# Kernel optimization log

Hardware: AMD Instinct MI355X
Metric: run time of the kernel (lower is better)

The kernel has to match this reference:

```python
import jax, jax.numpy as jnp
import numpy as np

IOU_THRESHOLD = 0.5
CLASS_CONF_THRESHOLD = 0.01
MAX_OUTPUT = 100  # tf.image.non_max_suppression max_output_size


def _nms_indices(boxes, scores, max_out, iou_thr):
    """Fixed-size greedy NMS: returns (idxs[max_out], valid[max_out])."""
    x1, y1, x2, y2 = boxes[:, 0], boxes[:, 1], boxes[:, 2], boxes[:, 3]
    areas = (x2 - x1) * (y2 - y1)

    def body(sc, _):
        i = jnp.argmax(sc)
        valid = sc[i] > 0.0  # score_threshold = 0.0 in tf call
        xx1 = jnp.maximum(x1[i], x1)
        yy1 = jnp.maximum(y1[i], y1)
        xx2 = jnp.minimum(x2[i], x2)
        yy2 = jnp.minimum(y2[i], y2)
        inter = jnp.maximum(xx2 - xx1, 0.0) * jnp.maximum(yy2 - yy1, 0.0)
        union = areas[i] + areas - inter
        iou = jnp.where(union > 0.0, inter / union, 0.0)
        # suppress overlapping boxes (self included, iou=1) only if pick valid
        sc_new = jnp.where((iou > iou_thr) & valid, -1.0, sc)
        return sc_new, (i, valid)

    _, (idxs, valids) = jax.lax.scan(body, scores, None, length=max_out)
    return idxs, valids


def _decode(x, anchors):
    B, H, W, A, C = x.shape  # B == 1
    gw = jnp.float32(W)
    # grid offsets: (col, row) per cell, matching cell_x / transposed cell_y
    cx = jnp.broadcast_to(jnp.arange(W, dtype=jnp.float32).reshape(1, 1, W, 1, 1), (1, H, W, 1, 1))
    cy = jnp.broadcast_to(jnp.arange(H, dtype=jnp.float32).reshape(1, H, 1, 1, 1), (1, H, W, 1, 1))
    grid = jnp.concatenate([cx, cy], axis=-1)  # (1,H,W,1,2)

    xy = (jax.nn.sigmoid(x[..., 0:2]) + grid) / gw                      # (B,H,W,A,2)
    wh = jnp.exp(x[..., 2:4]) * anchors.reshape(1, 1, 1, A, 2) / gw     # (B,H,W,A,2)
    boxes = jnp.concatenate([xy - wh / 2.0, xy + wh / 2.0], axis=-1)    # (B,H,W,A,4)

    conf = jax.nn.sigmoid(x[..., 4:5])                                  # (B,H,W,A,1)
    cls_prob = jax.nn.softmax(x[..., 5:], axis=-1)                      # (B,H,W,A,C-5)
    class_confidence = conf * cls_prob
    masked = jnp.where(class_confidence > CLASS_CONF_THRESHOLD, class_confidence, 0.0)
    classes = jnp.argmax(masked, axis=-1).astype(jnp.int32)             # (B,H,W,A)
    confm = jnp.max(masked, axis=-1)                                    # (B,H,W,A)

    N = H * W * A
    return boxes.reshape(N, 4), confm.reshape(N), classes.reshape(N)


def reference(x, anchors):
    boxes, scores, classes = _decode(x, anchors)
    idxs, valids = _nms_indices(jax.lax.stop_gradient(boxes),
                                jax.lax.stop_gradient(scores),
                                MAX_OUTPUT, IOU_THRESHOLD)
    sel_conf = jnp.where(valids, scores[idxs], 0.0)
    sel_boxes = jnp.where(valids[:, None], boxes[idxs], 0.0)
    sel_classes = jnp.where(valids, classes[idxs], -1)
    return sel_conf, sel_boxes, sel_classes


def setup_inputs() -> dict:
    key = jax.random.key(0)
    k1, k2 = jax.random.split(key)
    x = jax.random.normal(k1, (1, 256, 256, 5, 85), dtype=jnp.float32)
    # anchor priors in grid units (positive widths/heights)
    anchors = jax.random.uniform(k2, (5, 2), dtype=jnp.float32) * 4.0 + 0.5
    return {"x": x, "anchors": anchors}
```

## Files before the change

kernel.cpp:

```cpp
#include <hip/hip_runtime.h>
#include <hip/hip_bf16.h>

#define NROW 327680
#define NCLS 80
#define K_TARGET 1024u
#define CAP 2048u
#define MAX_OUT 100
#define NBIN 864
#define BIN0 0x3C23

#define WS_SCORES 0
#define WS_HIST   1310720
#define WS_CNT    1314176
#define WS_KEYS   1314240

typedef __attribute__((address_space(1))) const unsigned int g_uint;
typedef __attribute__((address_space(3))) unsigned int lds_uint;

__device__ __forceinline__ void async_copy16(const float* g, float* l) {
  __builtin_amdgcn_global_load_lds((const g_uint*)g, (lds_uint*)l, 16, 0, 0);
}

__global__ __launch_bounds__(64) void decode_score(
    const float* __restrict__ x, float* __restrict__ scores) {
  __shared__ float lds[64 * 85];
  const int t = threadIdx.x;
  const int row0 = blockIdx.x * 64;
  const float* gbase = x + (size_t)row0 * 85;

  #pragma unroll
  for (int i = 0; i < 21; ++i) {
    const int idx = i * 64 + t;
    async_copy16(gbase + idx * 4, lds + idx * 4);
  }
  if (t < 16) {
    const int idx = 1344 + t;
    async_copy16(gbase + idx * 4, lds + idx * 4);
  }
  __syncthreads();

  const float* row = lds + t * 85;
  float m = row[5];
  for (int c = 1; c < NCLS; ++c) { float l = row[5 + c]; if (l > m) m = l; }
  float s = 0.f;
  for (int c = 0; c < NCLS; ++c) s += expf(row[5 + c] - m);
  float conf = 1.f / (1.f + expf(-row[4]));
  float p = 1.f / s;
  float best = conf * p;
  scores[row0 + t] = (best > 0.01f) ? best : 0.f;
}

__global__ __launch_bounds__(1024) void hist_kernel(
    const float* __restrict__ scores, unsigned* __restrict__ hist) {
  __shared__ unsigned h[NBIN];
  const int t = threadIdx.x;
  if (t < NBIN) h[t] = 0;
  __syncthreads();

  float4 s4 = ((const float4*)scores)[blockIdx.x * 1024 + t];
  float sv[4] = {s4.x, s4.y, s4.z, s4.w};
  #pragma unroll
  for (int k = 0; k < 4; ++k) {
    float s = sv[k];
    if (s > 0.f) {
      int idx = (int)(__float_as_uint(s) >> 16) - BIN0;
      if (idx > NBIN - 1) idx = NBIN - 1;
      atomicAdd(&h[idx], 1u);
    }
  }
  __syncthreads();
  if (t < NBIN && h[t]) atomicAdd(&hist[t], h[t]);
}

__global__ __launch_bounds__(1024) void thresh_kernel(
    const unsigned* __restrict__ hist, unsigned* __restrict__ cnt) {
  __shared__ unsigned bufA[1024], bufB[1024];
  const int t = threadIdx.x;
  bufA[t] = (t < NBIN) ? hist[t] : 0u;
  __syncthreads();
  unsigned* src = bufA; unsigned* dst = bufB;
  for (int d = 1; d < 1024; d <<= 1) {
    unsigned val = src[t] + ((t + d < 1024) ? src[t + d] : 0u);
    dst[t] = val;
    __syncthreads();
    unsigned* tmp = src; src = dst; dst = tmp;
  }
  if (src[t] >= K_TARGET && (t == 1023 || src[t + 1] < K_TARGET)) {
    unsigned T = (unsigned)t;
    if (src[t] > CAP) T += 1;
    cnt[1] = T;
  }
  if (t == 0 && src[0] < K_TARGET) cnt[1] = 0;
}

__global__ __launch_bounds__(256) void compact_kernel(
    const float* __restrict__ scores, unsigned* __restrict__ cnt,
    unsigned long long* __restrict__ keys) {
  __shared__ unsigned blocal, bbase;
  const int t = threadIdx.x;
  if (t == 0) blocal = 0;
  __syncthreads();

  const unsigned T = cnt[1];
  const int gi = blockIdx.x * 256 + t;
  float4 s4 = ((const float4*)scores)[gi];
  float sv[4] = {s4.x, s4.y, s4.z, s4.w};
  unsigned long long lk[4]; int nl = 0;
  #pragma unroll
  for (int k = 0; k < 4; ++k) {
    float s = sv[k];
    if (s <= 0.f) continue;
    unsigned bits = __float_as_uint(s);
    int idx = (int)(bits >> 16) - BIN0;
    if (idx > NBIN - 1) idx = NBIN - 1;
    if ((unsigned)idx < T) continue;
    unsigned r = (unsigned)(gi * 4 + k);
    lk[nl++] = ((unsigned long long)bits << 32) |
               (unsigned long long)(0xFFFFFFFFu - r);
  }
  unsigned lpos = nl ? atomicAdd(&blocal, (unsigned)nl) : 0u;
  __syncthreads();
  if (t == 0 && blocal) bbase = atomicAdd(&cnt[0], blocal);
  __syncthreads();
  if (nl) {
    unsigned base = bbase + lpos;
    for (int i = 0; i < nl; ++i)
      if (base + i < CAP) keys[base + i] = lk[i];
  }
}

__global__ __launch_bounds__(1024) void final_kernel(
    const float* __restrict__ x, const float* __restrict__ anchors,
    const unsigned* __restrict__ cnt, const unsigned long long* __restrict__ keys,
    float* __restrict__ out) {
  __shared__ unsigned long long sk[CAP];
  __shared__ float4 cbox[CAP];
  __shared__ float4 kbox[MAX_OUT];
  __shared__ float  kscore[MAX_OUT];
  __shared__ int    krow[MAX_OUT];
  __shared__ int    knum;
  const int t = threadIdx.x;
  if (t == 0) knum = 0;

  unsigned n = cnt[0]; if (n > CAP) n = CAP;
  unsigned npow2 = 2; while (npow2 < n) npow2 <<= 1;
  for (unsigned i = t; i < npow2; i += 1024) sk[i] = (i < n) ? keys[i] : 0ull;
  __syncthreads();

  for (unsigned k = 2; k <= npow2; k <<= 1) {
    for (unsigned j = k >> 1; j > 0; j >>= 1) {
      for (unsigned i = t; i < npow2; i += 1024) {
        unsigned ixj = i ^ j;
        if (ixj > i) {
          unsigned long long a = sk[i], b = sk[ixj];
          bool desc = ((i & k) == 0);
          if (desc ? (a < b) : (a > b)) { sk[i] = b; sk[ixj] = a; }
        }
      }
      __syncthreads();
    }
  }

  for (unsigned i = t; i < n; i += 1024) {
    unsigned r = 0xFFFFFFFFu - (unsigned)(sk[i] & 0xFFFFFFFFull);
    const float* rp = x + (size_t)r * 85;
    float tx = rp[0], ty = rp[1], tw = rp[2], th = rp[3];
    const int a  = (int)(r % 5u);
    const int hw = (int)(r / 5u);
    const float wf = (float)(hw & 255);
    const float hf = (float)(hw >> 8);
    float sx = 1.f / (1.f + expf(-tx));
    float sy = 1.f / (1.f + expf(-ty));
    float xc = (sx + wf) / 256.f;
    float yc = (sy + hf) / 256.f;
    float bw = expf(tw) * anchors[2*a]     / 256.f;
    float bh = expf(th) * anchors[2*a + 1] / 256.f;
    float hwd = bw / 2.f, hhd = bh / 2.f;
    cbox[i] = make_float4(xc - hwd, yc - hhd, xc + hwd, yc + hhd);
  }
  __syncthreads();

  if (t < 64) {
    int nk = 0;
    float ax1=0,ay1=0,ax2=0,ay2=0,aar=0;
    float bx1=0,by1=0,bx2=0,by2=0,bar=0;
    for (unsigned cc = 0; cc < n && nk < MAX_OUT; ++cc) {
      unsigned long long key = sk[cc];
      unsigned sbits = (unsigned)(key >> 32);
      if (sbits == 0u) break;
      float4 bb = cbox[cc];
      float area = (bb.z - bb.x) * (bb.w - bb.y);
      bool s0 = false, s1 = false;
      if (t < nk) {
        float xx1 = fmaxf(ax1, bb.x), yy1 = fmaxf(ay1, bb.y);
        float xx2 = fminf(ax2, bb.z), yy2 = fminf(ay2, bb.w);
        float inter = fmaxf(xx2 - xx1, 0.f) * fmaxf(yy2 - yy1, 0.f);
        float uni = aar + area - inter;
        s0 = (uni > 0.f) && (inter / uni > 0.5f);
      }
      if (t + 64 < nk) {
        float xx1 = fmaxf(bx1, bb.x), yy1 = fmaxf(by1, bb.y);
        float xx2 = fminf(bx2, bb.z), yy2 = fminf(by2, bb.w);
        float inter = fmaxf(xx2 - xx1, 0.f) * fmaxf(yy2 - yy1, 0.f);
        float uni = bar + area - inter;
        s1 = (uni > 0.f) && (inter / uni > 0.5f);
      }
      if (!__any(s0 || s1)) {
        if (t == nk)      { ax1=bb.x; ay1=bb.y; ax2=bb.z; ay2=bb.w; aar=area; }
        if (t == nk - 64) { bx1=bb.x; by1=bb.y; bx2=bb.z; by2=bb.w; bar=area; }
        if (t == 0) {
          unsigned r = 0xFFFFFFFFu - (unsigned)(key & 0xFFFFFFFFull);
          kbox[nk] = bb; kscore[nk] = __uint_as_float(sbits); krow[nk] = (int)r;
        }
        ++nk;
      }
    }
    if (t == 0) knum = nk;
  }
  __syncthreads();

  if (t < MAX_OUT) {
    float conf = 0.f; float4 bb = make_float4(0.f, 0.f, 0.f, 0.f); float cf = -1.f;
    if (t < knum) {
      conf = kscore[t]; bb = kbox[t];
      const float* rp = x + (size_t)krow[t] * 85;
      float m = rp[5]; int am = 0;
      for (int c = 1; c < NCLS; ++c) { float l = rp[5 + c]; if (l > m) { m = l; am = c; } }
      cf = (float)am;
    }
    out[t] = conf;
    ((float4*)(out + 100))[t] = bb;
    out[500 + t] = cf;
  }
}

extern "C" void kernel_launch(void* const* d_in, const int* in_sizes, int n_in,
                              void* d_out, int out_size, void* d_ws, size_t ws_size,
                              hipStream_t stream) {
  const float* x       = (const float*)d_in[0];
  const float* anchors = (const float*)d_in[1];
  float* out = (float*)d_out;
  char* ws = (char*)d_ws;

  float*              scores = (float*)(ws + WS_SCORES);
  unsigned*           hist   = (unsigned*)(ws + WS_HIST);
  unsigned*           cnt    = (unsigned*)(ws + WS_CNT);
  unsigned long long* keys   = (unsigned long long*)(ws + WS_KEYS);

  hipMemsetAsync(hist, 0, NBIN * sizeof(unsigned) + 64, stream);

  hipLaunchKernelGGL(decode_score, dim3(NROW / 64), dim3(64),
                     0, stream, x, scores);
  hipLaunchKernelGGL(hist_kernel, dim3(NROW / 4096), dim3(1024),
                     0, stream, scores, hist);
  hipLaunchKernelGGL(thresh_kernel, dim3(1), dim3(1024), 0, stream, hist, cnt);
  hipLaunchKernelGGL(compact_kernel, dim3(NROW / 1024), dim3(256),
                     0, stream, scores, cnt, keys);
  hipLaunchKernelGGL(final_kernel, dim3(1), dim3(1024), 0, stream,
                     x, anchors, cnt, keys, out);
}
```

Baseline: 249.3 us.

## Register-load decode rows, per-block histograms, halve bitonic threads, parallel class argmax

The decode kernel stops staging rows through LDS with async copies and instead has each thread load its 85-float row straight into registers using unaligned vector loads, at 256 threads per block. Histogram blocks write per-block partials that the threshold kernel sums, which drops the memset and global atomics; the threshold kernel now also resets the compaction counter. Bitonic sort iterations give each thread one compare pair, with no idle half. The NMS loop prefetches the next key and box, and the per-keep class argmax runs wave-parallel with shuffles. Per-thread row loads are strided by 340 bytes and uncoalesced, and the 80-element register array may raise register pressure.

```diff
diff --git a/kernel.cpp b/kernel.cpp
--- a/kernel.cpp
+++ b/kernel.cpp
@@ -8,50 +8,42 @@
 #define MAX_OUT 100
 #define NBIN 864
 #define BIN0 0x3C23
+#define HIST_BLOCKS 80
 
 #define WS_SCORES 0
-#define WS_HIST   1310720
-#define WS_CNT    1314176
-#define WS_KEYS   1314240
-
-typedef __attribute__((address_space(1))) const unsigned int g_uint;
-typedef __attribute__((address_space(3))) unsigned int lds_uint;
-
-__device__ __forceinline__ void async_copy16(const float* g, float* l) {
-  __builtin_amdgcn_global_load_lds((const g_uint*)g, (lds_uint*)l, 16, 0, 0);
-}
-
-__global__ __launch_bounds__(64) void decode_score(
+#define WS_PART   1310720
+#define WS_CNT    1587200
+#define WS_KEYS   1587264
+
+typedef float f4v __attribute__((ext_vector_type(4)));
+typedef f4v f4u __attribute__((aligned(4)));
+
+__global__ __launch_bounds__(256, 1) void decode_score(
     const float* __restrict__ x, float* __restrict__ scores) {
-  __shared__ float lds[64 * 85];
-  const int t = threadIdx.x;
-  const int row0 = blockIdx.x * 64;
-  const float* gbase = x + (size_t)row0 * 85;
-
-  #pragma unroll
-  for (int i = 0; i < 21; ++i) {
-    const int idx = i * 64 + t;
-    async_copy16(gbase + idx * 4, lds + idx * 4);
-  }
-  if (t < 16) {
-    const int idx = 1344 + t;
-    async_copy16(gbase + idx * 4, lds + idx * 4);
-  }
-  __syncthreads();
-
-  const float* row = lds + t * 85;
-  float m = row[5];
-  for (int c = 1; c < NCLS; ++c) { float l = row[5 + c]; if (l > m) m = l; }
+  const int r = blockIdx.x * 256 + threadIdx.x;
+  const float* rp = x + (size_t)r * 85;
+
+  float conf_l = rp[4];
+  float cl[80];
+  #pragma unroll
+  for (int c = 0; c < 20; ++c) {
+    f4v t4 = *(const f4u*)(rp + 5 + 4 * c);
+    cl[4*c+0] = t4.x; cl[4*c+1] = t4.y; cl[4*c+2] = t4.z; cl[4*c+3] = t4.w;
+  }
+
+  float m = cl[0];
+  #pragma unroll
+  for (int c = 1; c < NCLS; ++c) { float l = cl[c]; if (l > m) m = l; }
   float s = 0.f;
-  for (int c = 0; c < NCLS; ++c) s += expf(row[5 + c] - m);
-  float conf = 1.f / (1.f + expf(-row[4]));
-  float p = 1.f / s;
-  float best = conf * p;
-  scores[row0 + t] = (best > 0.01f) ? best : 0.f;
+  #pragma unroll
+  for (int c = 0; c < NCLS; ++c) s += expf(cl[c] - m);
+  float conf = 1.f / (1.f + expf(-conf_l));
+  float best = conf * (1.f / s);
+  scores[r] = (best > 0.01f) ? best : 0.f;
 }
 
 __global__ __launch_bounds__(1024) void hist_kernel(
-    const float* __restrict__ scores, unsigned* __restrict__ hist) {
+    const float* __restrict__ scores, unsigned* __restrict__ part) {
   __shared__ unsigned h[NBIN];
   const int t = threadIdx.x;
   if (t < NBIN) h[t] = 0;
@@ -69,15 +61,29 @@
     }
   }
   __syncthreads();
-  if (t < NBIN && h[t]) atomicAdd(&hist[t], h[t]);
+  if (t < NBIN) part[blockIdx.x * NBIN + t] = h[t];
 }
 
 __global__ __launch_bounds__(1024) void thresh_kernel(
-    const unsigned* __restrict__ hist, unsigned* __restrict__ cnt) {
+    const unsigned* __restrict__ part, unsigned* __restrict__ cnt) {
   __shared__ unsigned bufA[1024], bufB[1024];
   const int t = threadIdx.x;
-  bufA[t] = (t < NBIN) ? hist[t] : 0u;
-  __syncthreads();
+
+  unsigned colsum = 0;
+  if (t < NBIN) {
+    unsigned a0 = 0, a1 = 0, a2 = 0, a3 = 0;
+    #pragma unroll
+    for (int b = 0; b < HIST_BLOCKS; b += 4) {
+      a0 += part[(b + 0) * NBIN + t];
+      a1 += part[(b + 1) * NBIN + t];
+      a2 += part[(b + 2) * NBIN + t];
+      a3 += part[(b + 3) * NBIN + t];
+    }
+    colsum = a0 + a1 + a2 + a3;
+  }
+  bufA[t] = colsum;
+  __syncthreads();
+
   unsigned* src = bufA; unsigned* dst = bufB;
   for (int d = 1; d < 1024; d <<= 1) {
     unsigned val = src[t] + ((t + d < 1024) ? src[t + d] : 0u);
@@ -90,7 +96,10 @@
     if (src[t] > CAP) T += 1;
     cnt[1] = T;
   }
-  if (t == 0 && src[0] < K_TARGET) cnt[1] = 0;
+  if (t == 0) {
+    if (src[0] < K_TARGET) cnt[1] = 0;
+    cnt[0] = 0;
+  }
 }
 
 __global__ __launch_bounds__(256) void compact_kernel(
@@ -138,6 +147,7 @@
   __shared__ float4 kbox[MAX_OUT];
   __shared__ float  kscore[MAX_OUT];
   __shared__ int    krow[MAX_OUT];
+  __shared__ int    kcls[MAX_OUT];
   __shared__ int    knum;
   const int t = threadIdx.x;
   if (t == 0) knum = 0;
@@ -149,13 +159,12 @@
 
   for (unsigned k = 2; k <= npow2; k <<= 1) {
     for (unsigned j = k >> 1; j > 0; j >>= 1) {
-      for (unsigned i = t; i < npow2; i += 1024) {
-        unsigned ixj = i ^ j;
-        if (ixj > i) {
-          unsigned long long a = sk[i], b = sk[ixj];
-          bool desc = ((i & k) == 0);
-          if (desc ? (a < b) : (a > b)) { sk[i] = b; sk[ixj] = a; }
-        }
+      for (unsigned p = t; p < (npow2 >> 1); p += 1024) {
+        unsigned i = ((p & ~(j - 1u)) << 1) | (p & (j - 1u));
+        unsigned ixj = i | j;
+        unsigned long long a = sk[i], b = sk[ixj];
+        bool desc = ((i & k) == 0);
+        if (desc ? (a < b) : (a > b)) { sk[i] = b; sk[ixj] = a; }
       }
       __syncthreads();
     }
@@ -184,11 +193,13 @@
     int nk = 0;
     float ax1=0,ay1=0,ax2=0,ay2=0,aar=0;
     float bx1=0,by1=0,bx2=0,by2=0,bar=0;
+    unsigned long long key = (n > 0) ? sk[0] : 0ull;
+    float4 bb = (n > 0) ? cbox[0] : make_float4(0,0,0,0);
     for (unsigned cc = 0; cc < n && nk < MAX_OUT; ++cc) {
-      unsigned long long key = sk[cc];
+      unsigned long long key_n = (cc + 1 < n) ? sk[cc + 1] : 0ull;
+      float4 bb_n = (cc + 1 < n) ? cbox[cc + 1] : make_float4(0,0,0,0);
       unsigned sbits = (unsigned)(key >> 32);
       if (sbits == 0u) break;
-      float4 bb = cbox[cc];
       float area = (bb.z - bb.x) * (bb.w - bb.y);
       bool s0 = false, s1 = false;
       if (t < nk) {
@@ -214,20 +225,44 @@
         }
         ++nk;
       }
+      key = key_n; bb = bb_n;
     }
     if (t == 0) knum = nk;
+  }
+  __syncthreads();
+
+  {
+    const int wv = t >> 6, lane = t & 63;
+    for (int kidx = wv; kidx < knum; kidx += 16) {
+      const float* rp = x + (size_t)krow[kidx] * 85;
+      float l0 = rp[5 + lane];
+      unsigned b0 = __float_as_uint(l0);
+      b0 = (b0 & 0x80000000u) ? ~b0 : (b0 | 0x80000000u);
+      unsigned long long kv =
+          ((unsigned long long)b0 << 32) | (unsigned long long)(0xFFFFFFFFu - lane);
+      if (lane < 16) {
+        float l1 = rp[5 + 64 + lane];
+        unsigned b1 = __float_as_uint(l1);
+        b1 = (b1 & 0x80000000u) ? ~b1 : (b1 | 0x80000000u);
+        unsigned long long kv1 =
+            ((unsigned long long)b1 << 32) |
+            (unsigned long long)(0xFFFFFFFFu - (64 + lane));
+        if (kv1 > kv) kv = kv1;
+      }
+      #pragma unroll
+      for (int d = 32; d >= 1; d >>= 1) {
+        unsigned long long o = __shfl_xor((long long)kv, d, 64);
+        if (o > kv) kv = o;
+      }
+      if (lane == 0)
+        kcls[kidx] = (int)(0xFFFFFFFFu - (unsigned)(kv & 0xFFFFFFFFull));
+    }
   }
   __syncthreads();
 
   if (t < MAX_OUT) {
     float conf = 0.f; float4 bb = make_float4(0.f, 0.f, 0.f, 0.f); float cf = -1.f;
-    if (t < knum) {
-      conf = kscore[t]; bb = kbox[t];
-      const float* rp = x + (size_t)krow[t] * 85;
-      float m = rp[5]; int am = 0;
-      for (int c = 1; c < NCLS; ++c) { float l = rp[5 + c]; if (l > m) { m = l; am = c; } }
-      cf = (float)am;
-    }
+    if (t < knum) { conf = kscore[t]; bb = kbox[t]; cf = (float)kcls[t]; }
     out[t] = conf;
     ((float4*)(out + 100))[t] = bb;
     out[500 + t] = cf;
@@ -243,17 +278,15 @@
   char* ws = (char*)d_ws;
 
   float*              scores = (float*)(ws + WS_SCORES);
-  unsigned*           hist   = (unsigned*)(ws + WS_HIST);
+  unsigned*           part   = (unsigned*)(ws + WS_PART);
   unsigned*           cnt    = (unsigned*)(ws + WS_CNT);
   unsigned long long* keys   = (unsigned long long*)(ws + WS_KEYS);
 
-  hipMemsetAsync(hist, 0, NBIN * sizeof(unsigned) + 64, stream);
-
-  hipLaunchKernelGGL(decode_score, dim3(NROW / 64), dim3(64),
+  hipLaunchKernelGGL(decode_score, dim3(NROW / 256), dim3(256),
                      0, stream, x, scores);
-  hipLaunchKernelGGL(hist_kernel, dim3(NROW / 4096), dim3(1024),
-                     0, stream, scores, hist);
-  hipLaunchKernelGGL(thresh_kernel, dim3(1), dim3(1024), 0, stream, hist, cnt);
+  hipLaunchKernelGGL(hist_kernel, dim3(HIST_BLOCKS), dim3(1024),
+                     0, stream, scores, part);
+  hipLaunchKernelGGL(thresh_kernel, dim3(1), dim3(1024), 0, stream, part, cnt);
   hipLaunchKernelGGL(compact_kernel, dim3(NROW / 1024), dim3(256),
                      0, stream, scores, cnt, keys);
   hipLaunchKernelGGL(final_kernel, dim3(1), dim3(1024), 0, stream,
```

Result: faster. 237.8 us (-4.6%).
